# Performance work log

Measured on AMD Instinct MI355X. Metric: run time of the kernel, lower is better.

Reference implementation:

```python
import jax, jax.numpy as jnp
import numpy as np

N_NODES = 20000
N_EDGES = 320000
L = 512   # input feature dim (size_dict['small'][0])
D = 256   # hidden dim (feat_channel), heads=1 so head_dim = 256
C = 2     # n_classes


def setup_inputs() -> dict:
    key = jax.random.key(0)
    ks = jax.random.split(key, 18)
    s = 0.02
    inp = {
        "x": jax.random.normal(ks[0], (N_NODES, L), jnp.float32),
        "edge_index": jax.random.randint(ks[1], (2, N_EDGES), 0, N_NODES, dtype=jnp.int32),
        "label": 1,
        # TransformerConv(L, D, heads=1): query/key/value + root skip projections
        "Wq": jax.random.normal(ks[2], (L, D), jnp.float32) * s,
        "bq": jax.random.normal(ks[3], (D,), jnp.float32) * s,
        "Wk": jax.random.normal(ks[4], (L, D), jnp.float32) * s,
        "bk": jax.random.normal(ks[5], (D,), jnp.float32) * s,
        "Wv": jax.random.normal(ks[6], (L, D), jnp.float32) * s,
        "bv": jax.random.normal(ks[7], (D,), jnp.float32) * s,
        "Ws": jax.random.normal(ks[8], (L, D), jnp.float32) * s,
        "bs": jax.random.normal(ks[9], (D,), jnp.float32) * s,
        # GlobalAdaptPooling: tanh-MLP attention (heads = n_classes) + per-class classifier
        "Wa1": jax.random.normal(ks[10], (D, D), jnp.float32) * s,
        "ba1": jax.random.normal(ks[11], (D,), jnp.float32) * s,
        "Wa2": jax.random.normal(ks[12], (D, C), jnp.float32) * s,
        "ba2": jax.random.normal(ks[13], (C,), jnp.float32) * s,
        "Wc": jax.random.normal(ks[14], (C, D), jnp.float32) * s,
        "bc": jax.random.normal(ks[15], (C,), jnp.float32) * s,
    }
    return inp


def _forward(x, edge_index, label, Wq, bq, Wk, bk, Wv, bv, Ws, bs, Wa1, ba1, Wa2, ba2, Wc, bc):
    n = x.shape[0]
    src = edge_index[0]  # message source j
    dst = edge_index[1]  # message target i
    # --- TransformerConv (heads=1, concat, root_weight=True) ---
    q = x @ Wq + bq                      # [N, D]
    k = x @ Wk + bk
    v = x @ Wv + bv
    score = jnp.sum(q[dst] * k[src], axis=-1) / jnp.sqrt(jnp.float32(D))  # [E]
    # segment softmax over incoming edges of each target node
    m = jax.ops.segment_max(score, dst, num_segments=n)
    e = jnp.exp(score - m[dst])
    den = jax.ops.segment_sum(e, dst, num_segments=n)
    alpha = e / den[dst]                 # [E]
    agg = jax.ops.segment_sum(alpha[:, None] * v[src], dst, num_segments=n)  # [N, D]
    h = agg + x @ Ws + bs
    # --- act: GELU (torch exact/erf) ---
    h = jax.nn.gelu(h, approximate=False)
    # --- GlobalAdaptPooling: node attention with n_classes heads ---
    scores = jnp.tanh(h @ Wa1 + ba1) @ Wa2 + ba2      # [N, C]
    attn = jax.nn.softmax(scores, axis=0)             # softmax over nodes
    M = attn.T @ h                                    # [C, D] per-class bag embedding
    logits = (jnp.sum(M * Wc, axis=1) + bc)[None, :]  # [1, C]
    Y_prob = jax.nn.softmax(logits, axis=1)
    A = attn[:, label]                                # [N] attention for target class
    return logits, Y_prob, A


def reference(x, edge_index, label, Wq, bq, Wk, bk, Wv, bv, Ws, bs, Wa1, ba1, Wa2, ba2, Wc, bc):
    return _forward(x, edge_index, label, Wq, bq, Wk, bk, Wv, bv, Ws, bs, Wa1, ba1, Wa2, ba2, Wc, bc)
```

## Files before the change

### kernel.cpp

```cpp
#include <hip/hip_runtime.h>
#include <hip/hip_bf16.h>
#include <math.h>

typedef float f32x4_t __attribute__((ext_vector_type(4)));
typedef float f32x2_t __attribute__((ext_vector_type(2)));
typedef __bf16 bf16x8_t __attribute__((ext_vector_type(8)));

__device__ __forceinline__ float bf2f(unsigned int u){
  union { float f; unsigned int i; } x; x.i = u << 16; return x.f;
}
__device__ __forceinline__ unsigned short f2bf(float f){
  unsigned int x = __float_as_uint(f);
  unsigned int r = (x + 0x7fffu + ((x >> 16) & 1u)) >> 16;
  return (unsigned short)r;
}
__device__ __forceinline__ unsigned int pk2bf(float a, float b){
  return (unsigned int)f2bf(a) | ((unsigned int)f2bf(b) << 16);
}
__device__ __forceinline__ int swz4(int r){ return (r ^ (r >> 2) ^ (r >> 4)) & 3; }

__device__ __forceinline__ void unp8s(uint4 w, float* f, float s){
  f[0] = bf2f(w.x & 0xffffu) * s; f[1] = bf2f(w.x >> 16) * s;
  f[2] = bf2f(w.y & 0xffffu) * s; f[3] = bf2f(w.y >> 16) * s;
  f[4] = bf2f(w.z & 0xffffu) * s; f[5] = bf2f(w.z >> 16) * s;
  f[6] = bf2f(w.w & 0xffffu) * s; f[7] = bf2f(w.w >> 16) * s;
}
__device__ __forceinline__ void unpf8(unsigned int w, float* f){
  f32x2_t lo = __builtin_amdgcn_cvt_pk_f32_fp8(w, false);
  f32x2_t hi = __builtin_amdgcn_cvt_pk_f32_fp8(w, true);
  f[0] = lo[0]; f[1] = lo[1]; f[2] = hi[0]; f[3] = hi[1];
}

#define GLOAD16(gsrc, ldst) \
  __builtin_amdgcn_global_load_lds((const __attribute__((address_space(1))) unsigned int*)(gsrc), \
                                   (__attribute__((address_space(3))) unsigned int*)(ldst), 16, 0, 0)

__global__ void pack_weights(const float* __restrict__ Wq, const float* __restrict__ Wk,
                             const float* __restrict__ Wv, const float* __restrict__ Ws,
                             const float* __restrict__ bq, const float* __restrict__ bk,
                             const float* __restrict__ bv, const float* __restrict__ bs,
                             unsigned short* __restrict__ wcatT, float* __restrict__ bcat){
  int idx = blockIdx.x * 256 + threadIdx.x;
  if (idx < 1024 * 512){
    int c = idx >> 9, k = idx & 511;
    int sel = c >> 8, cc = c & 255;
    const float* W = (sel == 0) ? Wq : (sel == 1) ? Wk : (sel == 2) ? Wv : Ws;
    int p = ((k >> 3) & 3) ^ swz4(c & 127);
    int dst = c * 512 + (k & ~31) + p * 8 + (k & 7);
    wcatT[dst] = f2bf(W[k * 256 + cc]);
  }
  if (idx < 1024){
    int sel = idx >> 8, cc = idx & 255;
    const float* B = (sel == 0) ? bq : (sel == 1) ? bk : (sel == 2) ? bv : bs;
    bcat[idx] = B[cc];
  }
}

__global__ void pack_wa1(const float* __restrict__ Wa1, unsigned short* __restrict__ wa1T){
  int idx = blockIdx.x * 256 + threadIdx.x;
  int c = idx >> 8, k = idx & 255;
  wa1T[idx] = f2bf(Wa1[k * 256 + c]);
}

__global__ void convert_x(const float* __restrict__ x, unsigned short* __restrict__ xbf, int nunits){
  int idx = blockIdx.x * 256 + threadIdx.x;
  if (idx >= nunits) return;
  int node = idx >> 6, un = idx & 63;
  int k0 = (un >> 2) * 32, u = un & 3;
  const float* src = x + (size_t)node * 512 + k0 + u * 8;
  float4 f0 = *reinterpret_cast<const float4*>(src);
  float4 f1 = *reinterpret_cast<const float4*>(src + 4);
  uint4 o;
  o.x = pk2bf(f0.x, f0.y); o.y = pk2bf(f0.z, f0.w);
  o.z = pk2bf(f1.x, f1.y); o.w = pk2bf(f1.z, f1.w);
  int p = u ^ swz4(node & 127);
  *reinterpret_cast<uint4*>(xbf + (size_t)node * 512 + k0 + p * 8) = o;
}

__global__ __launch_bounds__(256) void gemm_qkvs(const unsigned short* __restrict__ xbf,
                                                 const unsigned short* __restrict__ wcatT,
                                                 const float* __restrict__ bcat,
                                                 unsigned short* __restrict__ qbf,
                                                 unsigned short* __restrict__ sbf,
                                                 unsigned char* __restrict__ kv8,
                                                 int n_nodes, int mblocks){
  __shared__ __align__(16) unsigned char smem[32768];
  const int tid = threadIdx.x;
  const int lane = tid & 63, wave = tid >> 6;
  const int wm = wave >> 1, wn = wave & 1;
  const int g = (blockIdx.x & 7) * mblocks + (blockIdx.x >> 3);
  const int m_blk = g >> 3, n_blk = g & 7;
  const int m0 = m_blk * 128, n0 = n_blk * 128;
  const int lrow = lane >> 2;
  const int lcol = (lane & 3) * 8;
  const int rA0 = min(m0 + wave * 16 + lrow, n_nodes - 1);
  const int rA1 = min(m0 + (wave + 4) * 16 + lrow, n_nodes - 1);
  const int rB0 = n0 + wave * 16 + lrow;
  const int rB1 = rB0 + 64;
  const int r = lane & 15, q4 = lane >> 4;
  const unsigned short* aG0 = xbf   + (size_t)rA0 * 512 + lcol;
  const unsigned short* aG1 = xbf   + (size_t)rA1 * 512 + lcol;
  const unsigned short* bG0 = wcatT + (size_t)rB0 * 512 + lcol;
  const unsigned short* bG1 = wcatT + (size_t)rB1 * 512 + lcol;
  int aoff[4], boff[4];
  #pragma unroll
  for (int mi = 0; mi < 4; mi++){ int rr = wm * 64 + mi * 16 + r; aoff[mi] = rr * 32 + ((q4 ^ swz4(rr)) * 8); }
  #pragma unroll
  for (int ni = 0; ni < 4; ni++){ int rb = wn * 64 + ni * 16 + r; boff[ni] = rb * 32 + ((q4 ^ swz4(rb)) * 8); }
  f32x4_t acc[4][4] = {};
#define STAGE(buf, k0) { \
    unsigned short* As_ = (unsigned short*)(smem + (buf) * 16384); \
    unsigned short* Bs_ = (unsigned short*)(smem + (buf) * 16384 + 8192); \
    GLOAD16(aG0 + (k0), &As_[wave * 512]); \
    GLOAD16(aG1 + (k0), &As_[(wave + 4) * 512]); \
    GLOAD16(bG0 + (k0), &Bs_[wave * 512]); \
    GLOAD16(bG1 + (k0), &Bs_[(wave + 4) * 512]); \
  }
  STAGE(0, 0);
  int cur = 0;
  #pragma unroll 4
  for (int t = 0; t < 16; t++){
    if (t < 15){
      STAGE(cur ^ 1, (t + 1) * 32);
      asm volatile("s_waitcnt vmcnt(4)" ::: "memory");
    } else {
      asm volatile("s_waitcnt vmcnt(0)" ::: "memory");
    }
    __builtin_amdgcn_s_barrier();
    asm volatile("" ::: "memory");
    const unsigned short* As = (const unsigned short*)(smem + cur * 16384);
    const unsigned short* Bs = (const unsigned short*)(smem + cur * 16384 + 8192);
    bf16x8_t a[4], b[4];
    #pragma unroll
    for (int mi = 0; mi < 4; mi++) a[mi] = *reinterpret_cast<const bf16x8_t*>(&As[aoff[mi]]);
    #pragma unroll
    for (int ni = 0; ni < 4; ni++) b[ni] = *reinterpret_cast<const bf16x8_t*>(&Bs[boff[ni]]);
    #pragma unroll
    for (int mi = 0; mi < 4; mi++)
      #pragma unroll
      for (int ni = 0; ni < 4; ni++)
        acc[mi][ni] = __builtin_amdgcn_mfma_f32_16x16x32_bf16(b[ni], a[mi], acc[mi][ni], 0, 0, 0);
    __builtin_amdgcn_s_barrier();
    asm volatile("" ::: "memory");
    cur ^= 1;
  }
#undef STAGE
  const bool isQ = (n_blk < 2), isS = (n_blk >= 6);
  if (isQ || isS){
    unsigned short* St = (unsigned short*)smem;
    unsigned short* outp = isQ ? qbf : sbf;
    const int colhalf = isQ ? n_blk : (n_blk - 6);
    #pragma unroll
    for (int ch = 0; ch < 2; ch++){
      if (wm == ch){
        #pragma unroll
        for (int mi = 0; mi < 4; mi++){
          #pragma unroll
          for (int ni = 0; ni < 4; ni++){
            int mloc = mi * 16 + r;
            int nl = wn * 64 + ni * 16 + q4 * 4;
            float4 bb = *reinterpret_cast<const float4*>(&bcat[n0 + nl]);
            uint2 w;
            w.x = pk2bf(acc[mi][ni][0] + bb.x, acc[mi][ni][1] + bb.y);
            w.y = pk2bf(acc[mi][ni][2] + bb.z, acc[mi][ni][3] + bb.w);
            *reinterpret_cast<uint2*>(&St[mloc * 152 + nl]) = w;
          }
        }
      }
      __syncthreads();
      #pragma unroll
      for (int it = 0; it < 4; it++){
        int u = it * 256 + tid;
        int row = u >> 4, seg = (u & 15) * 8;
        int node = m0 + ch * 64 + row;
        if (node < n_nodes){
          uint4 v = *reinterpret_cast<const uint4*>(&St[row * 152 + seg]);
          *reinterpret_cast<uint4*>(outp + (size_t)node * 256 + colhalf * 128 + seg) = v;
        }
      }
      __syncthreads();
    }
  } else {
    unsigned char* St8 = smem;
    #pragma unroll
    for (int ch = 0; ch < 2; ch++){
      if (wm == ch){
        #pragma unroll
        for (int mi = 0; mi < 4; mi++){
          #pragma unroll
          for (int ni = 0; ni < 4; ni++){
            int mloc = mi * 16 + r;
            int nl = wn * 64 + ni * 16 + q4 * 4;
            float4 bb = *reinterpret_cast<const float4*>(&bcat[n0 + nl]);
            int u = 0;
            u = __builtin_amdgcn_cvt_pk_fp8_f32(acc[mi][ni][0] + bb.x, acc[mi][ni][1] + bb.y, u, false);
            u = __builtin_amdgcn_cvt_pk_fp8_f32(acc[mi][ni][2] + bb.z, acc[mi][ni][3] + bb.w, u, true);
            *reinterpret_cast<unsigned int*>(&St8[mloc * 144 + nl]) = (unsigned int)u;
          }
        }
      }
      __syncthreads();
      #pragma unroll
      for (int it = 0; it < 2; it++){
        int u = it * 256 + tid;
        int row = u >> 3, seg = (u & 7) * 16;
        int node = m0 + ch * 64 + row;
        if (node < n_nodes){
          uint4 v = *reinterpret_cast<const uint4*>(&St8[row * 144 + seg]);
          *reinterpret_cast<uint4*>(kv8 + (size_t)node * 512 + (n_blk - 2) * 128 + seg) = v;
        }
      }
      __syncthreads();
    }
  }
}

__global__ void degree_hist(const int* __restrict__ ei, int* __restrict__ deg, int ne){
  int i = blockIdx.x * 256 + threadIdx.x;
  if (i < ne) atomicAdd(&deg[ei[ne + i]], 1);
}

__global__ void scan_deg(const int* __restrict__ deg, int* __restrict__ rowstart, int n, int ne){
  __shared__ int sm[1024];
  int tid = threadIdx.x;
  int per = (n + 1023) / 1024;
  int start = tid * per;
  int sum = 0;
  for (int i = 0; i < per; i++){
    int idx = start + i;
    sum += (idx < n) ? deg[idx] : 0;
  }
  sm[tid] = sum; __syncthreads();
  for (int off = 1; off < 1024; off <<= 1){
    int t = (tid >= off) ? sm[tid - off] : 0;
    __syncthreads();
    sm[tid] += t;
    __syncthreads();
  }
  int run = sm[tid] - sum;
  for (int i = 0; i < per; i++){
    int idx = start + i;
    if (idx < n){
      rowstart[idx] = run;
      run += deg[idx];
    }
  }
  if (tid == 0) rowstart[n] = ne;
}

__global__ void scatter_edges(const int* __restrict__ ei, const int* __restrict__ rowstart,
                              int* __restrict__ cursor, int* __restrict__ csrsrc, int ne){
  int i = blockIdx.x * 256 + threadIdx.x;
  if (i < ne){
    int d = ei[ne + i];
    int pos = atomicAdd(&cursor[d], 1);
    csrsrc[rowstart[d] + pos] = ei[i] << 9;
  }
}

__global__ __launch_bounds__(256) void edge_attn(const unsigned short* __restrict__ qbf,
                                                 const unsigned short* __restrict__ sbf,
                                                 const unsigned char* __restrict__ kv8,
                                                 const int* __restrict__ rowstart,
                                                 const int* __restrict__ csrsrc,
                                                 unsigned short* __restrict__ hbf, int n_nodes){
  const int tid = threadIdx.x;
  const int lane = tid & 63, wave = tid >> 6;
  const int g = lane >> 4, t = lane & 15;
  const int node = blockIdx.x * 16 + wave * 4 + g;
  const bool active = node < n_nodes;
  const int nd = active ? node : 0;
  const float qs = 0.0625f * 1.44269504088896340736f;
  float q[16];
  {
    const unsigned short* qp = qbf + (size_t)nd * 256 + t * 16;
    uint4 w0 = *reinterpret_cast<const uint4*>(qp);
    uint4 w1 = *reinterpret_cast<const uint4*>(qp + 8);
    unp8s(w0, q, qs); unp8s(w1, q + 8, qs);
  }
  int rs = rowstart[nd];
  int re = active ? rowstart[nd + 1] : rs;
  float m = -1e30f, den = 0.f;
  float acc[16];
  #pragma unroll
  for (int j = 0; j < 16; j++) acc[j] = 0.f;
  uint4 kw, vw;
  if (rs < re){
    const unsigned char* kb = kv8 + (size_t)csrsrc[rs] + t * 16;
    kw = *reinterpret_cast<const uint4*>(kb);
    vw = *reinterpret_cast<const uint4*>(kb + 256);
  }
  for (int i = rs; i < re; i++){
    uint4 kwc = kw, vwc = vw;
    if (i + 1 < re){
      const unsigned char* kb = kv8 + (size_t)csrsrc[i + 1] + t * 16;
      kw = *reinterpret_cast<const uint4*>(kb);
      vw = *reinterpret_cast<const uint4*>(kb + 256);
    }
    float kf[16];
    unpf8(kwc.x, kf); unpf8(kwc.y, kf + 4); unpf8(kwc.z, kf + 8); unpf8(kwc.w, kf + 12);
    float s = 0.f;
    #pragma unroll
    for (int j = 0; j < 16; j++) s = fmaf(q[j], kf[j], s);
    s += __shfl_xor(s, 1); s += __shfl_xor(s, 2);
    s += __shfl_xor(s, 4); s += __shfl_xor(s, 8);
    float vf[16];
    unpf8(vwc.x, vf); unpf8(vwc.y, vf + 4); unpf8(vwc.z, vf + 8); unpf8(vwc.w, vf + 12);
    float mn = fmaxf(m, s);
    float sc = exp2f(m - mn);
    float e  = exp2f(s - mn);
    den = den * sc + e;
    #pragma unroll
    for (int j = 0; j < 16; j++) acc[j] = fmaf(acc[j], sc, e * vf[j]);
    m = mn;
  }
  float inv = (den > 0.f) ? 1.f / den : 0.f;
  const unsigned short* sp = sbf + (size_t)nd * 256 + t * 16;
  uint4 s0 = *reinterpret_cast<const uint4*>(sp);
  uint4 s1 = *reinterpret_cast<const uint4*>(sp + 8);
  float sf[16]; unp8s(s0, sf, 1.0f); unp8s(s1, sf + 8, 1.0f);
  const float inv_sqrt2 = 0.70710678118654752f;
  unsigned int o[8];
  #pragma unroll
  for (int j = 0; j < 8; j++){
    float h0 = acc[2 * j] * inv + sf[2 * j];
    float h1 = acc[2 * j + 1] * inv + sf[2 * j + 1];
    h0 = 0.5f * h0 * (1.f + erff(h0 * inv_sqrt2));
    h1 = 0.5f * h1 * (1.f + erff(h1 * inv_sqrt2));
    o[j] = (unsigned int)f2bf(h0) | ((unsigned int)f2bf(h1) << 16);
  }
  if (active){
    uint4* dst = reinterpret_cast<uint4*>(hbf + (size_t)node * 256 + t * 16);
    dst[0] = make_uint4(o[0], o[1], o[2], o[3]);
    dst[1] = make_uint4(o[4], o[5], o[6], o[7]);
  }
}

__global__ __launch_bounds__(256) void mlp_mfma(const unsigned short* __restrict__ hbf,
                                                const unsigned short* __restrict__ wa1T,
                                                const float* __restrict__ ba1,
                                                const float* __restrict__ Wa2,
                                                const float* __restrict__ ba2,
                                                float* __restrict__ s2, int n_nodes){
  __shared__ __align__(16) unsigned short As[64 * 72];
  __shared__ float s2s[64][2];
  const int tid = threadIdx.x;
  const int lane = tid & 63, wave = tid >> 6;
  const int m0 = blockIdx.x * 64;
  const int c0 = wave * 64;
  const int r = lane & 15, rg = (lane >> 4) * 4;
  if (tid < 128) s2s[tid >> 1][tid & 1] = 0.f;
  f32x4_t acc[4][4] = {};
  for (int k0 = 0; k0 < 256; k0 += 64){
    int arow = tid >> 2, akc = (tid & 3) * 16;
    uint4 a0v = make_uint4(0,0,0,0), a1v = make_uint4(0,0,0,0);
    if (m0 + arow < n_nodes){
      const unsigned short* src = hbf + (size_t)(m0 + arow) * 256 + k0 + akc;
      a0v = *reinterpret_cast<const uint4*>(src);
      a1v = *reinterpret_cast<const uint4*>(src + 8);
    }
    *reinterpret_cast<uint4*>(&As[arow * 72 + akc]) = a0v;
    *reinterpret_cast<uint4*>(&As[arow * 72 + akc + 8]) = a1v;
    __syncthreads();
    #pragma unroll
    for (int kk = 0; kk < 2; kk++){
      int kg = kk * 32 + (lane >> 4) * 8;
      bf16x8_t a[4], b[4];
      #pragma unroll
      for (int mi = 0; mi < 4; mi++)
        a[mi] = *reinterpret_cast<const bf16x8_t*>(&As[(mi * 16 + r) * 72 + kg]);
      #pragma unroll
      for (int ni = 0; ni < 4; ni++)
        b[ni] = *reinterpret_cast<const bf16x8_t*>(wa1T + (size_t)(c0 + ni * 16 + r) * 256 + k0 + kg);
      #pragma unroll
      for (int mi = 0; mi < 4; mi++)
        #pragma unroll
        for (int ni = 0; ni < 4; ni++)
          acc[mi][ni] = __builtin_amdgcn_mfma_f32_16x16x32_bf16(a[mi], b[ni], acc[mi][ni], 0, 0, 0);
    }
    __syncthreads();
  }
  float w20[4], w21[4], b1c[4];
  #pragma unroll
  for (int ni = 0; ni < 4; ni++){
    int col = c0 + ni * 16 + r;
    w20[ni] = Wa2[col * 2]; w21[ni] = Wa2[col * 2 + 1]; b1c[ni] = ba1[col];
  }
  #pragma unroll
  for (int mi = 0; mi < 4; mi++){
    #pragma unroll
    for (int j = 0; j < 4; j++){
      float t0 = 0.f, t1 = 0.f;
      #pragma unroll
      for (int ni = 0; ni < 4; ni++){
        float t = tanhf(acc[mi][ni][j] + b1c[ni]);
        t0 += t * w20[ni]; t1 += t * w21[ni];
      }
      t0 += __shfl_xor(t0, 1); t0 += __shfl_xor(t0, 2);
      t0 += __shfl_xor(t0, 4); t0 += __shfl_xor(t0, 8);
      t1 += __shfl_xor(t1, 1); t1 += __shfl_xor(t1, 2);
      t1 += __shfl_xor(t1, 4); t1 += __shfl_xor(t1, 8);
      if (r == 0){
        int row = mi * 16 + rg + j;
        atomicAdd(&s2s[row][0], t0);
        atomicAdd(&s2s[row][1], t1);
      }
    }
  }
  __syncthreads();
  if (tid < 128){
    int row = tid >> 1, c = tid & 1;
    int node = m0 + row;
    if (node < n_nodes) s2[node * 2 + c] = s2s[row][c] + ba2[c];
  }
}

__global__ void col_reduce(const float* __restrict__ s2, float* __restrict__ red, int n){
  __shared__ float sm[1024];
  __shared__ float mshare[2];
  int tid = threadIdx.x;
  float mx0 = -INFINITY, mx1 = -INFINITY;
  for (int i = tid; i < n; i += 1024){
    mx0 = fmaxf(mx0, s2[2 * i]);
    mx1 = fmaxf(mx1, s2[2 * i + 1]);
  }
  sm[tid] = mx0; __syncthreads();
  for (int off = 512; off > 0; off >>= 1){
    if (tid < off) sm[tid] = fmaxf(sm[tid], sm[tid + off]);
    __syncthreads();
  }
  if (tid == 0) mshare[0] = sm[0];
  __syncthreads();
  sm[tid] = mx1; __syncthreads();
  for (int off = 512; off > 0; off >>= 1){
    if (tid < off) sm[tid] = fmaxf(sm[tid], sm[tid + off]);
    __syncthreads();
  }
  if (tid == 0) mshare[1] = sm[0];
  __syncthreads();
  float m0 = mshare[0], m1 = mshare[1];
  float s0 = 0.f, s1 = 0.f;
  for (int i = tid; i < n; i += 1024){
    s0 += expf(s2[2 * i] - m0);
    s1 += expf(s2[2 * i + 1] - m1);
  }
  sm[tid] = s0; __syncthreads();
  for (int off = 512; off > 0; off >>= 1){
    if (tid < off) sm[tid] += sm[tid + off];
    __syncthreads();
  }
  float den0 = sm[0];
  __syncthreads();
  sm[tid] = s1; __syncthreads();
  for (int off = 512; off > 0; off >>= 1){
    if (tid < off) sm[tid] += sm[tid + off];
    __syncthreads();
  }
  if (tid == 0){
    red[0] = m0; red[1] = m1; red[2] = den0; red[3] = sm[0];
  }
}

__global__ __launch_bounds__(256) void attn_M(const float* __restrict__ s2, const float* __restrict__ red,
                                              const unsigned short* __restrict__ hbf, const int* __restrict__ label,
                                              float* __restrict__ Mbuf, float* __restrict__ outA, int n){
  __shared__ float a0s[256], a1s[256];
  int tid = threadIdx.x;
  int n0 = blockIdx.x * 256;
  int node = n0 + tid;
  float m0 = red[0], m1 = red[1];
  float i0 = 1.f / red[2], i1 = 1.f / red[3];
  float a0 = 0.f, a1 = 0.f;
  if (node < n){
    a0 = expf(s2[2 * node] - m0) * i0;
    a1 = expf(s2[2 * node + 1] - m1) * i1;
    outA[node] = (label[0] == 0) ? a0 : a1;
  }
  a0s[tid] = a0; a1s[tid] = a1;
  __syncthreads();
  int d = tid;
  float M0 = 0.f, M1 = 0.f;
  int cnt = min(256, n - n0);
  for (int i = 0; i < cnt; i++){
    float hv = bf2f((unsigned int)hbf[(size_t)(n0 + i) * 256 + d]);
    M0 += a0s[i] * hv;
    M1 += a1s[i] * hv;
  }
  atomicAdd(&Mbuf[d], M0);
  atomicAdd(&Mbuf[256 + d], M1);
}

__global__ void final_k(const float* __restrict__ Mbuf, const float* __restrict__ Wc,
                        const float* __restrict__ bc, float* __restrict__ out){
  __shared__ float sm[256];
  __shared__ float l0s;
  int tid = threadIdx.x;
  float p0 = Mbuf[tid] * Wc[tid];
  float p1 = Mbuf[256 + tid] * Wc[256 + tid];
  sm[tid] = p0; __syncthreads();
  for (int off = 128; off > 0; off >>= 1){
    if (tid < off) sm[tid] += sm[tid + off];
    __syncthreads();
  }
  if (tid == 0) l0s = sm[0];
  __syncthreads();
  sm[tid] = p1; __syncthreads();
  for (int off = 128; off > 0; off >>= 1){
    if (tid < off) sm[tid] += sm[tid + off];
    __syncthreads();
  }
  if (tid == 0){
    float l0 = l0s + bc[0];
    float l1 = sm[0] + bc[1];
    out[0] = l0; out[1] = l1;
    float mx = fmaxf(l0, l1);
    float e0 = expf(l0 - mx), e1 = expf(l1 - mx);
    float inv = 1.f / (e0 + e1);
    out[2] = e0 * inv; out[3] = e1 * inv;
  }
}

extern "C" void kernel_launch(void* const* d_in, const int* in_sizes, int n_in,
                              void* d_out, int out_size, void* d_ws, size_t ws_size,
                              hipStream_t stream) {
  const float* x   = (const float*)d_in[0];
  const int*   ei  = (const int*)d_in[1];
  const int*   lab = (const int*)d_in[2];
  const float* Wq  = (const float*)d_in[3];
  const float* bq  = (const float*)d_in[4];
  const float* Wk  = (const float*)d_in[5];
  const float* bk  = (const float*)d_in[6];
  const float* Wv  = (const float*)d_in[7];
  const float* bv  = (const float*)d_in[8];
  const float* Ws  = (const float*)d_in[9];
  const float* bs  = (const float*)d_in[10];
  const float* Wa1 = (const float*)d_in[11];
  const float* ba1 = (const float*)d_in[12];
  const float* Wa2 = (const float*)d_in[13];
  const float* ba2 = (const float*)d_in[14];
  const float* Wc  = (const float*)d_in[15];
  const float* bc  = (const float*)d_in[16];
  float* out = (float*)d_out;

  const int n  = in_sizes[0] / 512;
  const int ne = in_sizes[1] / 2;

  char* ws = (char*)d_ws;
  size_t off = 0;
  auto take = [&](size_t bytes){ size_t r = off; off += (bytes + 255) & ~(size_t)255; return r; };
  unsigned short* wcatT  = (unsigned short*)(ws + take((size_t)1024 * 512 * 2));
  float*          bcat   = (float*)(ws + take(1024 * 4));
  unsigned short* xbf    = (unsigned short*)(ws + take((size_t)n * 512 * 2));
  unsigned short* qbf    = (unsigned short*)(ws + take((size_t)n * 256 * 2));
  unsigned short* sbf    = (unsigned short*)(ws + take((size_t)n * 256 * 2));
  unsigned char*  kv8    = (unsigned char*)(ws + take((size_t)n * 512));
  unsigned short* hbf    = (unsigned short*)(ws + take((size_t)n * 256 * 2));
  unsigned short* wa1T   = (unsigned short*)(ws + take((size_t)256 * 256 * 2));
  float*          s2     = (float*)(ws + take((size_t)n * 2 * 4));
  size_t zoff = off;
  int*            deg    = (int*)(ws + take((size_t)n * 4));
  int*            cursor = (int*)(ws + take((size_t)n * 4));
  float*          Mbuf   = (float*)(ws + take(512 * 4));
  size_t zlen = off - zoff;
  int*            rowst  = (int*)(ws + take((size_t)(n + 1) * 4));
  int*            csrsrc = (int*)(ws + take((size_t)ne * 4));
  float*          red    = (float*)(ws + take(4 * 4));

  hipMemsetAsync(ws + zoff, 0, zlen, stream);

  pack_weights<<<(1024 * 512 + 255) / 256, 256, 0, stream>>>(Wq, Wk, Wv, Ws, bq, bk, bv, bs, wcatT, bcat);
  pack_wa1<<<256, 256, 0, stream>>>(Wa1, wa1T);
  convert_x<<<(n * 64 + 255) / 256, 256, 0, stream>>>(x, xbf, n * 64);
  const int mblocks = (n + 127) / 128;
  gemm_qkvs<<<8 * mblocks, 256, 0, stream>>>(xbf, wcatT, bcat, qbf, sbf, kv8, n, mblocks);
  degree_hist<<<(ne + 255) / 256, 256, 0, stream>>>(ei, deg, ne);
  scan_deg<<<1, 1024, 0, stream>>>(deg, rowst, n, ne);
  scatter_edges<<<(ne + 255) / 256, 256, 0, stream>>>(ei, rowst, cursor, csrsrc, ne);
  edge_attn<<<(n + 15) / 16, 256, 0, stream>>>(qbf, sbf, kv8, rowst, csrsrc, hbf, n);
  mlp_mfma<<<(n + 63) / 64, 256, 0, stream>>>(hbf, wa1T, ba1, Wa2, ba2, s2, n);
  col_reduce<<<1, 1024, 0, stream>>>(s2, red, n);
  attn_M<<<(n + 255) / 256, 256, 0, stream>>>(s2, red, hbf, lab, Mbuf, out + 4, n);
  final_k<<<1, 256, 0, stream>>>(Mbuf, Wc, bc, out);
  (void)ws_size; (void)out_size; (void)n_in;
}
```

Baseline: 211.5 us.

## Merge prep kernels, triple-buffer GEMM loads, unroll edge attention by two

Folds the weight packing, Wa1 packing, x conversion and degree histogram into one prep launch, which removes several kernel launches and their serialization gaps. The QKVS GEMM moves from a double-buffered to a triple-buffered LDS pipeline (48KB shared memory) so loads run two K-steps ahead, which may lower occupancy. The edge attention loop now handles two edges per iteration, with paired prefetch and a joint online-softmax update, to expose more memory-level parallelism.

New measurement: 197.6 us. -6.6%, faster.

```diff
diff --git a/kernel.cpp b/kernel.cpp
--- a/kernel.cpp
+++ b/kernel.cpp
@@ -35,46 +35,51 @@
   __builtin_amdgcn_global_load_lds((const __attribute__((address_space(1))) unsigned int*)(gsrc), \
                                    (__attribute__((address_space(3))) unsigned int*)(ldst), 16, 0, 0)
 
-__global__ void pack_weights(const float* __restrict__ Wq, const float* __restrict__ Wk,
-                             const float* __restrict__ Wv, const float* __restrict__ Ws,
-                             const float* __restrict__ bq, const float* __restrict__ bk,
-                             const float* __restrict__ bv, const float* __restrict__ bs,
-                             unsigned short* __restrict__ wcatT, float* __restrict__ bcat){
-  int idx = blockIdx.x * 256 + threadIdx.x;
-  if (idx < 1024 * 512){
+__global__ void prep(const float* __restrict__ x,
+                     const float* __restrict__ Wq, const float* __restrict__ Wk,
+                     const float* __restrict__ Wv, const float* __restrict__ Ws,
+                     const float* __restrict__ bq, const float* __restrict__ bk,
+                     const float* __restrict__ bv, const float* __restrict__ bs,
+                     const float* __restrict__ Wa1, const int* __restrict__ ei,
+                     unsigned short* __restrict__ xbf, unsigned short* __restrict__ wcatT,
+                     float* __restrict__ bcat, unsigned short* __restrict__ wa1T,
+                     int* __restrict__ deg, int n, int ne, int nbcv){
+  const int b = blockIdx.x, tid = threadIdx.x;
+  if (b < 2048){
+    int idx = b * 256 + tid;
     int c = idx >> 9, k = idx & 511;
     int sel = c >> 8, cc = c & 255;
     const float* W = (sel == 0) ? Wq : (sel == 1) ? Wk : (sel == 2) ? Wv : Ws;
     int p = ((k >> 3) & 3) ^ swz4(c & 127);
     int dst = c * 512 + (k & ~31) + p * 8 + (k & 7);
     wcatT[dst] = f2bf(W[k * 256 + cc]);
-  }
-  if (idx < 1024){
-    int sel = idx >> 8, cc = idx & 255;
-    const float* B = (sel == 0) ? bq : (sel == 1) ? bk : (sel == 2) ? bv : bs;
-    bcat[idx] = B[cc];
-  }
-}
-
-__global__ void pack_wa1(const float* __restrict__ Wa1, unsigned short* __restrict__ wa1T){
-  int idx = blockIdx.x * 256 + threadIdx.x;
-  int c = idx >> 8, k = idx & 255;
-  wa1T[idx] = f2bf(Wa1[k * 256 + c]);
-}
-
-__global__ void convert_x(const float* __restrict__ x, unsigned short* __restrict__ xbf, int nunits){
-  int idx = blockIdx.x * 256 + threadIdx.x;
-  if (idx >= nunits) return;
-  int node = idx >> 6, un = idx & 63;
-  int k0 = (un >> 2) * 32, u = un & 3;
-  const float* src = x + (size_t)node * 512 + k0 + u * 8;
-  float4 f0 = *reinterpret_cast<const float4*>(src);
-  float4 f1 = *reinterpret_cast<const float4*>(src + 4);
-  uint4 o;
-  o.x = pk2bf(f0.x, f0.y); o.y = pk2bf(f0.z, f0.w);
-  o.z = pk2bf(f1.x, f1.y); o.w = pk2bf(f1.z, f1.w);
-  int p = u ^ swz4(node & 127);
-  *reinterpret_cast<uint4*>(xbf + (size_t)node * 512 + k0 + p * 8) = o;
+    if (idx < 1024){
+      int sel2 = idx >> 8, cc2 = idx & 255;
+      const float* B = (sel2 == 0) ? bq : (sel2 == 1) ? bk : (sel2 == 2) ? bv : bs;
+      bcat[idx] = B[cc2];
+    }
+  } else if (b < 2304){
+    int idx = (b - 2048) * 256 + tid;
+    int c = idx >> 8, k = idx & 255;
+    wa1T[idx] = f2bf(Wa1[k * 256 + c]);
+  } else if (b < 2304 + nbcv){
+    int idx = (b - 2304) * 256 + tid;
+    if (idx < n * 64){
+      int node = idx >> 6, un = idx & 63;
+      int k0 = (un >> 2) * 32, u = un & 3;
+      const float* src = x + (size_t)node * 512 + k0 + u * 8;
+      float4 f0 = *reinterpret_cast<const float4*>(src);
+      float4 f1 = *reinterpret_cast<const float4*>(src + 4);
+      uint4 o;
+      o.x = pk2bf(f0.x, f0.y); o.y = pk2bf(f0.z, f0.w);
+      o.z = pk2bf(f1.x, f1.y); o.w = pk2bf(f1.z, f1.w);
+      int p = u ^ swz4(node & 127);
+      *reinterpret_cast<uint4*>(xbf + (size_t)node * 512 + k0 + p * 8) = o;
+    }
+  } else {
+    int i = (b - 2304 - nbcv) * 256 + tid;
+    if (i < ne) atomicAdd(&deg[ei[ne + i]], 1);
+  }
 }
 
 __global__ __launch_bounds__(256) void gemm_qkvs(const unsigned short* __restrict__ xbf,
@@ -84,7 +89,7 @@
                                                  unsigned short* __restrict__ sbf,
                                                  unsigned char* __restrict__ kv8,
                                                  int n_nodes, int mblocks){
-  __shared__ __align__(16) unsigned char smem[32768];
+  __shared__ __align__(16) unsigned char smem[49152];
   const int tid = threadIdx.x;
   const int lane = tid & 63, wave = tid >> 6;
   const int wm = wave >> 1, wn = wave & 1;
@@ -108,28 +113,31 @@
   #pragma unroll
   for (int ni = 0; ni < 4; ni++){ int rb = wn * 64 + ni * 16 + r; boff[ni] = rb * 32 + ((q4 ^ swz4(rb)) * 8); }
   f32x4_t acc[4][4] = {};
-#define STAGE(buf, k0) { \
-    unsigned short* As_ = (unsigned short*)(smem + (buf) * 16384); \
-    unsigned short* Bs_ = (unsigned short*)(smem + (buf) * 16384 + 8192); \
+#define STAGE(base, k0) { \
+    unsigned short* As_ = (unsigned short*)(smem + (base)); \
+    unsigned short* Bs_ = (unsigned short*)(smem + (base) + 8192); \
     GLOAD16(aG0 + (k0), &As_[wave * 512]); \
     GLOAD16(aG1 + (k0), &As_[(wave + 4) * 512]); \
     GLOAD16(bG0 + (k0), &Bs_[wave * 512]); \
     GLOAD16(bG1 + (k0), &Bs_[(wave + 4) * 512]); \
   }
   STAGE(0, 0);
-  int cur = 0;
-  #pragma unroll 4
+  STAGE(16384, 32);
+  int cbase = 0;
+  int sbase = 32768;
   for (int t = 0; t < 16; t++){
-    if (t < 15){
-      STAGE(cur ^ 1, (t + 1) * 32);
+    if (t + 2 < 16){
+      STAGE(sbase, (t + 2) * 32);
+      asm volatile("s_waitcnt vmcnt(8)" ::: "memory");
+    } else if (t + 1 < 16){
       asm volatile("s_waitcnt vmcnt(4)" ::: "memory");
     } else {
       asm volatile("s_waitcnt vmcnt(0)" ::: "memory");
     }
     __builtin_amdgcn_s_barrier();
     asm volatile("" ::: "memory");
-    const unsigned short* As = (const unsigned short*)(smem + cur * 16384);
-    const unsigned short* Bs = (const unsigned short*)(smem + cur * 16384 + 8192);
+    const unsigned short* As = (const unsigned short*)(smem + cbase);
+    const unsigned short* Bs = (const unsigned short*)(smem + cbase + 8192);
     bf16x8_t a[4], b[4];
     #pragma unroll
     for (int mi = 0; mi < 4; mi++) a[mi] = *reinterpret_cast<const bf16x8_t*>(&As[aoff[mi]]);
@@ -142,7 +150,8 @@
         acc[mi][ni] = __builtin_amdgcn_mfma_f32_16x16x32_bf16(b[ni], a[mi], acc[mi][ni], 0, 0, 0);
     __builtin_amdgcn_s_barrier();
     asm volatile("" ::: "memory");
-    cur ^= 1;
+    cbase += 16384; if (cbase == 49152) cbase = 0;
+    sbase += 16384; if (sbase == 49152) sbase = 0;
   }
 #undef STAGE
   const bool isQ = (n_blk < 2), isS = (n_blk >= 6);
@@ -215,11 +224,6 @@
   }
 }
 
-__global__ void degree_hist(const int* __restrict__ ei, int* __restrict__ deg, int ne){
-  int i = blockIdx.x * 256 + threadIdx.x;
-  if (i < ne) atomicAdd(&deg[ei[ne + i]], 1);
-}
-
 __global__ void scan_deg(const int* __restrict__ deg, int* __restrict__ rowstart, int n, int ne){
   __shared__ int sm[1024];
   int tid = threadIdx.x;
@@ -284,41 +288,59 @@
   float acc[16];
   #pragma unroll
   for (int j = 0; j < 16; j++) acc[j] = 0.f;
-  uint4 kw, vw;
+  uint4 kA = make_uint4(0,0,0,0), vA = kA, kB = kA, vB = kA;
   if (rs < re){
-    const unsigned char* kb = kv8 + (size_t)csrsrc[rs] + t * 16;
-    kw = *reinterpret_cast<const uint4*>(kb);
-    vw = *reinterpret_cast<const uint4*>(kb + 256);
-  }
-  for (int i = rs; i < re; i++){
-    uint4 kwc = kw, vwc = vw;
-    if (i + 1 < re){
-      const unsigned char* kb = kv8 + (size_t)csrsrc[i + 1] + t * 16;
-      kw = *reinterpret_cast<const uint4*>(kb);
-      vw = *reinterpret_cast<const uint4*>(kb + 256);
-    }
-    float kf[16];
-    unpf8(kwc.x, kf); unpf8(kwc.y, kf + 4); unpf8(kwc.z, kf + 8); unpf8(kwc.w, kf + 12);
-    float s = 0.f;
-    #pragma unroll
-    for (int j = 0; j < 16; j++) s = fmaf(q[j], kf[j], s);
-    s += __shfl_xor(s, 1); s += __shfl_xor(s, 2);
-    s += __shfl_xor(s, 4); s += __shfl_xor(s, 8);
-    float vf[16];
-    unpf8(vwc.x, vf); unpf8(vwc.y, vf + 4); unpf8(vwc.z, vf + 8); unpf8(vwc.w, vf + 12);
-    float mn = fmaxf(m, s);
+    const unsigned char* p1 = kv8 + (size_t)csrsrc[rs] + t * 16;
+    kA = *reinterpret_cast<const uint4*>(p1);
+    vA = *reinterpret_cast<const uint4*>(p1 + 256);
+    if (rs + 1 < re){
+      const unsigned char* p2 = kv8 + (size_t)csrsrc[rs + 1] + t * 16;
+      kB = *reinterpret_cast<const uint4*>(p2);
+      vB = *reinterpret_cast<const uint4*>(p2 + 256);
+    }
+  }
+  for (int i = rs; i < re; i += 2){
+    uint4 k1 = kA, v1 = vA, k2 = kB, v2 = vB;
+    const bool has2 = (i + 1 < re);
+    if (i + 2 < re){
+      const unsigned char* p1 = kv8 + (size_t)csrsrc[i + 2] + t * 16;
+      kA = *reinterpret_cast<const uint4*>(p1);
+      vA = *reinterpret_cast<const uint4*>(p1 + 256);
+      if (i + 3 < re){
+        const unsigned char* p2 = kv8 + (size_t)csrsrc[i + 3] + t * 16;
+        kB = *reinterpret_cast<const uint4*>(p2);
+        vB = *reinterpret_cast<const uint4*>(p2 + 256);
+      }
+    }
+    float kf1[16], kf2[16];
+    unpf8(k1.x, kf1); unpf8(k1.y, kf1 + 4); unpf8(k1.z, kf1 + 8); unpf8(k1.w, kf1 + 12);
+    unpf8(k2.x, kf2); unpf8(k2.y, kf2 + 4); unpf8(k2.z, kf2 + 8); unpf8(k2.w, kf2 + 12);
+    float s1 = 0.f, s2 = 0.f;
+    #pragma unroll
+    for (int j = 0; j < 16; j++){ s1 = fmaf(q[j], kf1[j], s1); s2 = fmaf(q[j], kf2[j], s2); }
+    s1 += __shfl_xor(s1, 1); s2 += __shfl_xor(s2, 1);
+    s1 += __shfl_xor(s1, 2); s2 += __shfl_xor(s2, 2);
+    s1 += __shfl_xor(s1, 4); s2 += __shfl_xor(s2, 4);
+    s1 += __shfl_xor(s1, 8); s2 += __shfl_xor(s2, 8);
+    if (!has2) s2 = -1e30f;
+    float vf1[16], vf2[16];
+    unpf8(v1.x, vf1); unpf8(v1.y, vf1 + 4); unpf8(v1.z, vf1 + 8); unpf8(v1.w, vf1 + 12);
+    unpf8(v2.x, vf2); unpf8(v2.y, vf2 + 4); unpf8(v2.z, vf2 + 8); unpf8(v2.w, vf2 + 12);
+    float mn = fmaxf(m, fmaxf(s1, s2));
     float sc = exp2f(m - mn);
-    float e  = exp2f(s - mn);
-    den = den * sc + e;
-    #pragma unroll
-    for (int j = 0; j < 16; j++) acc[j] = fmaf(acc[j], sc, e * vf[j]);
+    float e1 = exp2f(s1 - mn);
+    float e2 = exp2f(s2 - mn);
+    den = den * sc + e1 + e2;
+    #pragma unroll
+    for (int j = 0; j < 16; j++)
+      acc[j] = fmaf(acc[j], sc, fmaf(e1, vf1[j], e2 * vf2[j]));
     m = mn;
   }
   float inv = (den > 0.f) ? 1.f / den : 0.f;
   const unsigned short* sp = sbf + (size_t)nd * 256 + t * 16;
   uint4 s0 = *reinterpret_cast<const uint4*>(sp);
-  uint4 s1 = *reinterpret_cast<const uint4*>(sp + 8);
-  float sf[16]; unp8s(s0, sf, 1.0f); unp8s(s1, sf + 8, 1.0f);
+  uint4 s1v = *reinterpret_cast<const uint4*>(sp + 8);
+  float sf[16]; unp8s(s0, sf, 1.0f); unp8s(s1v, sf + 8, 1.0f);
   const float inv_sqrt2 = 0.70710678118654752f;
   unsigned int o[8];
   #pragma unroll
@@ -568,12 +590,12 @@
 
   hipMemsetAsync(ws + zoff, 0, zlen, stream);
 
-  pack_weights<<<(1024 * 512 + 255) / 256, 256, 0, stream>>>(Wq, Wk, Wv, Ws, bq, bk, bv, bs, wcatT, bcat);
-  pack_wa1<<<256, 256, 0, stream>>>(Wa1, wa1T);
-  convert_x<<<(n * 64 + 255) / 256, 256, 0, stream>>>(x, xbf, n * 64);
+  const int nbcv = (n * 64 + 255) / 256;
+  const int nbdh = (ne + 255) / 256;
+  prep<<<2304 + nbcv + nbdh, 256, 0, stream>>>(x, Wq, Wk, Wv, Ws, bq, bk, bv, bs, Wa1, ei,
+                                               xbf, wcatT, bcat, wa1T, deg, n, ne, nbcv);
   const int mblocks = (n + 127) / 128;
   gemm_qkvs<<<8 * mblocks, 256, 0, stream>>>(xbf, wcatT, bcat, qbf, sbf, kv8, n, mblocks);
-  degree_hist<<<(ne + 255) / 256, 256, 0, stream>>>(ei, deg, ne);
   scan_deg<<<1, 1024, 0, stream>>>(deg, rowst, n, ne);
   scatter_edges<<<(ne + 255) / 256, 256, 0, stream>>>(ei, rowst, cursor, csrsrc, ne);
   edge_attn<<<(n + 15) / 16, 256, 0, stream>>>(qbf, sbf, kv8, rowst, csrsrc, hbf, n);
```
